# Optimization experiments

Measured on AMD Instinct MI355X. Metric: run time of the kernel, lower is better.

The kernel has to match this reference:

```python
import jax, jax.numpy as jnp
import numpy as np

N = 200000          # graph_size (stalk rows)
H = 128             # hidden_channels
NNZ = 3200000       # Laplacian nnz (avg degree 16)
K = 15              # polynomial degree (poly_layers_K)
LAMBDA_MAX = 2.0    # normalised Laplacian -> analytic lambda_max


def setup_inputs() -> dict:
    key = jax.random.key(0)
    ks = jax.random.split(key, 6)
    x = jax.random.normal(ks[0], (N, H), dtype=jnp.float32)
    vals = jax.random.normal(ks[1], (NNZ,), dtype=jnp.float32)
    poly_logits = jax.random.normal(ks[2], (K + 1,), dtype=jnp.float32)
    hp_alpha = jax.random.normal(ks[3], (), dtype=jnp.float32)
    edge_row = jax.random.randint(ks[4], (NNZ,), 0, N, dtype=jnp.int64)
    edge_col = jax.random.randint(ks[5], (NNZ,), 0, N, dtype=jnp.int64)
    return {"x": x, "vals": vals, "poly_logits": poly_logits,
            "hp_alpha": hp_alpha, "edge_row": edge_row, "edge_col": edge_col}


def reference(x, vals, poly_logits, hp_alpha, edge_row, edge_col):
    n = x.shape[0]

    def spmm(v):  # (n,h) -> (n,h), sparse L @ v in COO form
        return jax.ops.segment_sum(vals[:, None] * v[edge_col], edge_row,
                                   num_segments=n)

    def Lhat(v):  # L_hat = (2/lambda_max) L - I
        return (2.0 / LAMBDA_MAX) * spmm(v) - v

    w = jax.nn.softmax(poly_logits)  # mixture over Chebyshev T_0..T_K

    # Chebyshev Type-1 recurrence: T_{k+1} = 2 L_hat T_k - T_{k-1}
    T0 = x
    T1 = Lhat(x)
    out = w[0] * T0 + w[1] * T1

    def step(carry, wk):
        T0, T1, out = carry
        Tk1 = 2.0 * Lhat(T1) - T0
        return (T1, Tk1, out + wk * Tk1), None

    (_, _, px), _ = jax.lax.scan(step, (T0, T1, out), w[2:])

    # high-pass term: x - (1/lambda_max) L x
    hp = x - spmm(x) / LAMBDA_MAX
    return -px + hp_alpha * hp
```

## Files before the change

### kernel.cpp

```cpp
#include <hip/hip_runtime.h>
#include <math.h>

#define N_NODES 200000
#define H_CH    128
#define GRP     64
#define NNZ_E   3200000
#define K_DEG   15

__global__ void softmax_k(const float* __restrict__ logits, float* __restrict__ w) {
    if (threadIdx.x == 0) {
        float m = -1e30f;
        for (int i = 0; i <= K_DEG; ++i) m = fmaxf(m, logits[i]);
        float e[K_DEG + 1];
        float s = 0.f;
        for (int i = 0; i <= K_DEG; ++i) { e[i] = expf(logits[i] - m); s += e[i]; }
        float inv = 1.0f / s;
        for (int i = 0; i <= K_DEG; ++i) w[i] = e[i] * inv;
    }
}

__global__ void hist_k(const int* __restrict__ row, int* __restrict__ counts, int nnz) {
    int i = blockIdx.x * blockDim.x + threadIdx.x;
    if (i < nnz) atomicAdd(&counts[row[i]], 1);
}

__global__ void scan1_k(const int* __restrict__ counts, int* __restrict__ out,
                        int* __restrict__ partials, int n) {
    __shared__ int sm[256];
    int tbase = blockIdx.x * 2048 + threadIdx.x * 8;
    int v[8];
    int tsum = 0;
#pragma unroll
    for (int j = 0; j < 8; ++j) {
        int i = tbase + j;
        int c = (i < n) ? counts[i] : 0;
        v[j] = tsum;
        tsum += c;
    }
    sm[threadIdx.x] = tsum;
    __syncthreads();
    int incl = tsum;
    for (int off = 1; off < 256; off <<= 1) {
        int t = (threadIdx.x >= (unsigned)off) ? sm[threadIdx.x - off] : 0;
        __syncthreads();
        incl += t;
        sm[threadIdx.x] = incl;
        __syncthreads();
    }
    int texcl = incl - tsum;
    if (threadIdx.x == 255) partials[blockIdx.x] = incl;
#pragma unroll
    for (int j = 0; j < 8; ++j) {
        int i = tbase + j;
        if (i < n) out[i] = texcl + v[j];
    }
}

__global__ void scan2_k(int* partials, int nb, int* row_ptr, int n, int total) {
    __shared__ int sm[128];
    int v = (threadIdx.x < (unsigned)nb) ? partials[threadIdx.x] : 0;
    sm[threadIdx.x] = v;
    __syncthreads();
    int incl = v;
    for (int off = 1; off < 128; off <<= 1) {
        int t = (threadIdx.x >= (unsigned)off) ? sm[threadIdx.x - off] : 0;
        __syncthreads();
        incl += t;
        sm[threadIdx.x] = incl;
        __syncthreads();
    }
    if (threadIdx.x < (unsigned)nb) partials[threadIdx.x] = incl - v;
    if (threadIdx.x == 0) row_ptr[n] = total;
}

__global__ void scan3_k(int* __restrict__ row_ptr, const int* __restrict__ partials,
                        int* __restrict__ fill, int n) {
    int off = partials[blockIdx.x];
    int tbase = blockIdx.x * 2048 + threadIdx.x * 8;
#pragma unroll
    for (int j = 0; j < 8; ++j) {
        int i = tbase + j;
        if (i < n) {
            int v = row_ptr[i] + off;
            row_ptr[i] = v;
            fill[i] = v;
        }
    }
}

__global__ void scatter_k(const int* __restrict__ row, const int* __restrict__ col,
                          const float* __restrict__ vals, int* __restrict__ fill,
                          int2* __restrict__ csr, int nnz) {
    int i = blockIdx.x * blockDim.x + threadIdx.x;
    if (i < nnz) {
        int r = row[i];
        int p = atomicAdd(&fill[r], 1);
        int2 cv;
        cv.x = col[i];
        cv.y = __float_as_int(vals[i]);
        csr[p] = cv;
    }
}

__global__ __launch_bounds__(256) void first_k(
    const int* __restrict__ rp, const int2* __restrict__ csr,
    const float* __restrict__ x, float* __restrict__ T1g, float* __restrict__ out,
    const float* __restrict__ w, const float* __restrict__ alpha_p, int goff) {
    int wid = blockIdx.x * 4 + (threadIdx.x >> 6);
    int r = __builtin_amdgcn_readfirstlane(wid);
    if (r >= N_NODES) return;
    int lane = threadIdx.x & 63;
    const float* base = x + goff + lane;
    int e0 = rp[r], e1 = rp[r + 1];
    float a0 = 0.f, a1 = 0.f, a2 = 0.f, a3 = 0.f;
    int e = e0;
    for (; e + 4 <= e1; e += 4) {
        int2 cv0 = csr[e], cv1 = csr[e + 1], cv2 = csr[e + 2], cv3 = csr[e + 3];
        a0 = fmaf(__int_as_float(cv0.y), base[(size_t)cv0.x * H_CH], a0);
        a1 = fmaf(__int_as_float(cv1.y), base[(size_t)cv1.x * H_CH], a1);
        a2 = fmaf(__int_as_float(cv2.y), base[(size_t)cv2.x * H_CH], a2);
        a3 = fmaf(__int_as_float(cv3.y), base[(size_t)cv3.x * H_CH], a3);
    }
    for (; e < e1; ++e) {
        int2 cv = csr[e];
        a0 = fmaf(__int_as_float(cv.y), base[(size_t)cv.x * H_CH], a0);
    }
    float s = (a0 + a1) + (a2 + a3);
    size_t idxg = (size_t)r * GRP + lane;
    size_t idxf = (size_t)r * H_CH + goff + lane;
    float xr = x[idxf];
    float w0 = w[0], w1 = w[1], al = alpha_p[0];
    float t1 = s - xr;
    float o = -(w0 * xr + w1 * t1) + al * (xr - 0.5f * s);
    T1g[idxg] = t1;
    out[idxf] = o;
}

__global__ __launch_bounds__(256) void cheb_k(
    const int* __restrict__ rp, const int2* __restrict__ csr,
    const float* __restrict__ Tcur, const float* TprevBase, int tprevStride,
    float* Tnext, float* __restrict__ out,
    const float* __restrict__ w, int k, int goff) {
    int wid = blockIdx.x * 4 + (threadIdx.x >> 6);
    int r = __builtin_amdgcn_readfirstlane(wid);
    if (r >= N_NODES) return;
    int lane = threadIdx.x & 63;
    const float* base = Tcur + lane;
    int e0 = rp[r], e1 = rp[r + 1];
    float a0 = 0.f, a1 = 0.f, a2 = 0.f, a3 = 0.f;
    int e = e0;
    for (; e + 4 <= e1; e += 4) {
        int2 cv0 = csr[e], cv1 = csr[e + 1], cv2 = csr[e + 2], cv3 = csr[e + 3];
        a0 = fmaf(__int_as_float(cv0.y), base[(size_t)cv0.x * GRP], a0);
        a1 = fmaf(__int_as_float(cv1.y), base[(size_t)cv1.x * GRP], a1);
        a2 = fmaf(__int_as_float(cv2.y), base[(size_t)cv2.x * GRP], a2);
        a3 = fmaf(__int_as_float(cv3.y), base[(size_t)cv3.x * GRP], a3);
    }
    for (; e < e1; ++e) {
        int2 cv = csr[e];
        a0 = fmaf(__int_as_float(cv.y), base[(size_t)cv.x * GRP], a0);
    }
    float s = (a0 + a1) + (a2 + a3);
    size_t idxg = (size_t)r * GRP + lane;
    size_t idxf = (size_t)r * H_CH + goff + lane;
    float tc = Tcur[idxg];
    float tp = TprevBase[(size_t)r * tprevStride + lane];
    float wk = w[k];
    float tn = 2.0f * (s - tc) - tp;
    float o = out[idxf];
    o -= wk * tn;
    out[idxf] = o;
    Tnext[idxg] = tn;
}

extern "C" void kernel_launch(void* const* d_in, const int* in_sizes, int n_in,
                              void* d_out, int out_size, void* d_ws, size_t ws_size,
                              hipStream_t stream) {
    const float* x      = (const float*)d_in[0];
    const float* vals   = (const float*)d_in[1];
    const float* logits = (const float*)d_in[2];
    const float* alpha  = (const float*)d_in[3];
    const int*   erow   = (const int*)d_in[4];
    const int*   ecol   = (const int*)d_in[5];
    float* out = (float*)d_out;

    const size_t NG = (size_t)N_NODES * GRP;
    float* bufA    = (float*)d_ws;
    float* bufB    = bufA + NG;
    int2*  csr     = (int2*)(bufB + NG);
    int*   row_ptr = (int*)(csr + NNZ_E);
    int*   counts  = row_ptr + (N_NODES + 1);
    int*   fill    = counts + N_NODES;
    int*   partials= fill + N_NODES;
    float* w_buf   = (float*)(partials + 128);

    hipMemsetAsync(counts, 0, N_NODES * sizeof(int), stream);
    softmax_k<<<1, 64, 0, stream>>>(logits, w_buf);
    hist_k<<<(NNZ_E + 255) / 256, 256, 0, stream>>>(erow, counts, NNZ_E);

    const int TILE = 2048;
    int nblk = (N_NODES + TILE - 1) / TILE;
    scan1_k<<<nblk, 256, 0, stream>>>(counts, row_ptr, partials, N_NODES);
    scan2_k<<<1, 128, 0, stream>>>(partials, nblk, row_ptr, N_NODES, NNZ_E);
    scan3_k<<<nblk, 256, 0, stream>>>(row_ptr, partials, fill, N_NODES);
    scatter_k<<<(NNZ_E + 255) / 256, 256, 0, stream>>>(erow, ecol, vals, fill, csr, NNZ_E);

    int grid = (N_NODES + 3) / 4;

    for (int g = 0; g < H_CH / GRP; ++g) {
        int goff = g * GRP;
        first_k<<<grid, 256, 0, stream>>>(row_ptr, csr, x, bufB, out, w_buf, alpha, goff);
        cheb_k<<<grid, 256, 0, stream>>>(row_ptr, csr, bufB, x + goff, H_CH, bufA,
                                         out, w_buf, 2, goff);
        float* Tcur = bufA;
        float* Tprev = bufB;
        for (int k = 3; k <= K_DEG; ++k) {
            cheb_k<<<grid, 256, 0, stream>>>(row_ptr, csr, Tcur, Tprev, GRP, Tprev,
                                             out, w_buf, k, goff);
            float* t = Tcur; Tcur = Tprev; Tprev = t;
        }
    }
}
```

Before: 4.703 ms.

## Sort rows by degree, precompute scatter ranks, unroll SpMM gather by eight

Records each edge's rank within its row during the histogram pass, so the scatter no longer needs a second atomic pass over a fill array. Adds a degree bucketing pass that builds a permutation ordering rows from high to low degree, and the SpMM kernels process rows in that order to balance wave work. Widens the inner gather loop to eight independent accumulators for more loads in flight. In exchange, the permuted row order loses locality in the output and T writes, and the new rank buffer adds extra memory traffic.

```diff
diff --git a/kernel.cpp b/kernel.cpp
--- a/kernel.cpp
+++ b/kernel.cpp
@@ -6,6 +6,7 @@
 #define GRP     64
 #define NNZ_E   3200000
 #define K_DEG   15
+#define DEG_BINS 64
 
 __global__ void softmax_k(const float* __restrict__ logits, float* __restrict__ w) {
     if (threadIdx.x == 0) {
@@ -19,9 +20,10 @@
     }
 }
 
-__global__ void hist_k(const int* __restrict__ row, int* __restrict__ counts, int nnz) {
-    int i = blockIdx.x * blockDim.x + threadIdx.x;
-    if (i < nnz) atomicAdd(&counts[row[i]], 1);
+__global__ void rank_k(const int* __restrict__ row, int* __restrict__ counts,
+                       int* __restrict__ rank, int nnz) {
+    int i = blockIdx.x * blockDim.x + threadIdx.x;
+    if (i < nnz) rank[i] = atomicAdd(&counts[row[i]], 1);
 }
 
 __global__ void scan1_k(const int* __restrict__ counts, int* __restrict__ out,
@@ -73,28 +75,23 @@
     if (threadIdx.x == 0) row_ptr[n] = total;
 }
 
-__global__ void scan3_k(int* __restrict__ row_ptr, const int* __restrict__ partials,
-                        int* __restrict__ fill, int n) {
+__global__ void scan3_k(int* __restrict__ row_ptr, const int* __restrict__ partials, int n) {
     int off = partials[blockIdx.x];
     int tbase = blockIdx.x * 2048 + threadIdx.x * 8;
 #pragma unroll
     for (int j = 0; j < 8; ++j) {
         int i = tbase + j;
-        if (i < n) {
-            int v = row_ptr[i] + off;
-            row_ptr[i] = v;
-            fill[i] = v;
-        }
-    }
-}
-
-__global__ void scatter_k(const int* __restrict__ row, const int* __restrict__ col,
-                          const float* __restrict__ vals, int* __restrict__ fill,
-                          int2* __restrict__ csr, int nnz) {
+        if (i < n) row_ptr[i] += off;
+    }
+}
+
+__global__ void scatter2_k(const int* __restrict__ row, const int* __restrict__ col,
+                           const float* __restrict__ vals, const int* __restrict__ rank,
+                           const int* __restrict__ row_ptr, int2* __restrict__ csr, int nnz) {
     int i = blockIdx.x * blockDim.x + threadIdx.x;
     if (i < nnz) {
         int r = row[i];
-        int p = atomicAdd(&fill[r], 1);
+        int p = row_ptr[r] + rank[i];
         int2 cv;
         cv.x = col[i];
         cv.y = __float_as_int(vals[i]);
@@ -102,30 +99,75 @@
     }
 }
 
+__global__ void dhist_k(const int* __restrict__ counts, int* __restrict__ dhist, int n) {
+    __shared__ int h[DEG_BINS];
+    if (threadIdx.x < DEG_BINS) h[threadIdx.x] = 0;
+    __syncthreads();
+    int i = blockIdx.x * blockDim.x + threadIdx.x;
+    if (i < n) {
+        int d = counts[i];
+        int b = (d < DEG_BINS) ? (DEG_BINS - 1 - d) : 0;
+        atomicAdd(&h[b], 1);
+    }
+    __syncthreads();
+    if (threadIdx.x < DEG_BINS) atomicAdd(&dhist[threadIdx.x], h[threadIdx.x]);
+}
+
+__global__ void dscan_k(const int* __restrict__ dhist, int* __restrict__ dbase) {
+    if (threadIdx.x == 0) {
+        int s = 0;
+        for (int b = 0; b < DEG_BINS; ++b) { dbase[b] = s; s += dhist[b]; }
+    }
+}
+
+__global__ void dperm_k(const int* __restrict__ counts, const int* __restrict__ dbase,
+                        int* __restrict__ dcount, int* __restrict__ perm, int n) {
+    int i = blockIdx.x * blockDim.x + threadIdx.x;
+    if (i < n) {
+        int d = counts[i];
+        int b = (d < DEG_BINS) ? (DEG_BINS - 1 - d) : 0;
+        int p = dbase[b] + atomicAdd(&dcount[b], 1);
+        perm[p] = i;
+    }
+}
+
 __global__ __launch_bounds__(256) void first_k(
-    const int* __restrict__ rp, const int2* __restrict__ csr,
+    const int* __restrict__ rp, const int2* __restrict__ csr, const int* __restrict__ perm,
     const float* __restrict__ x, float* __restrict__ T1g, float* __restrict__ out,
     const float* __restrict__ w, const float* __restrict__ alpha_p, int goff) {
     int wid = blockIdx.x * 4 + (threadIdx.x >> 6);
-    int r = __builtin_amdgcn_readfirstlane(wid);
-    if (r >= N_NODES) return;
+    if (wid >= N_NODES) return;
+    int r = __builtin_amdgcn_readfirstlane(perm[wid]);
     int lane = threadIdx.x & 63;
     const float* base = x + goff + lane;
     int e0 = rp[r], e1 = rp[r + 1];
     float a0 = 0.f, a1 = 0.f, a2 = 0.f, a3 = 0.f;
+    float a4 = 0.f, a5 = 0.f, a6 = 0.f, a7 = 0.f;
     int e = e0;
+    for (; e + 8 <= e1; e += 8) {
+        int2 c0 = csr[e],     c1 = csr[e + 1], c2 = csr[e + 2], c3 = csr[e + 3];
+        int2 c4 = csr[e + 4], c5 = csr[e + 5], c6 = csr[e + 6], c7 = csr[e + 7];
+        a0 = fmaf(__int_as_float(c0.y), base[(size_t)c0.x * H_CH], a0);
+        a1 = fmaf(__int_as_float(c1.y), base[(size_t)c1.x * H_CH], a1);
+        a2 = fmaf(__int_as_float(c2.y), base[(size_t)c2.x * H_CH], a2);
+        a3 = fmaf(__int_as_float(c3.y), base[(size_t)c3.x * H_CH], a3);
+        a4 = fmaf(__int_as_float(c4.y), base[(size_t)c4.x * H_CH], a4);
+        a5 = fmaf(__int_as_float(c5.y), base[(size_t)c5.x * H_CH], a5);
+        a6 = fmaf(__int_as_float(c6.y), base[(size_t)c6.x * H_CH], a6);
+        a7 = fmaf(__int_as_float(c7.y), base[(size_t)c7.x * H_CH], a7);
+    }
     for (; e + 4 <= e1; e += 4) {
-        int2 cv0 = csr[e], cv1 = csr[e + 1], cv2 = csr[e + 2], cv3 = csr[e + 3];
-        a0 = fmaf(__int_as_float(cv0.y), base[(size_t)cv0.x * H_CH], a0);
-        a1 = fmaf(__int_as_float(cv1.y), base[(size_t)cv1.x * H_CH], a1);
-        a2 = fmaf(__int_as_float(cv2.y), base[(size_t)cv2.x * H_CH], a2);
-        a3 = fmaf(__int_as_float(cv3.y), base[(size_t)cv3.x * H_CH], a3);
+        int2 c0 = csr[e], c1 = csr[e + 1], c2 = csr[e + 2], c3 = csr[e + 3];
+        a0 = fmaf(__int_as_float(c0.y), base[(size_t)c0.x * H_CH], a0);
+        a1 = fmaf(__int_as_float(c1.y), base[(size_t)c1.x * H_CH], a1);
+        a2 = fmaf(__int_as_float(c2.y), base[(size_t)c2.x * H_CH], a2);
+        a3 = fmaf(__int_as_float(c3.y), base[(size_t)c3.x * H_CH], a3);
     }
     for (; e < e1; ++e) {
         int2 cv = csr[e];
         a0 = fmaf(__int_as_float(cv.y), base[(size_t)cv.x * H_CH], a0);
     }
-    float s = (a0 + a1) + (a2 + a3);
+    float s = ((a0 + a1) + (a2 + a3)) + ((a4 + a5) + (a6 + a7));
     size_t idxg = (size_t)r * GRP + lane;
     size_t idxf = (size_t)r * H_CH + goff + lane;
     float xr = x[idxf];
@@ -137,30 +179,43 @@
 }
 
 __global__ __launch_bounds__(256) void cheb_k(
-    const int* __restrict__ rp, const int2* __restrict__ csr,
+    const int* __restrict__ rp, const int2* __restrict__ csr, const int* __restrict__ perm,
     const float* __restrict__ Tcur, const float* TprevBase, int tprevStride,
     float* Tnext, float* __restrict__ out,
     const float* __restrict__ w, int k, int goff) {
     int wid = blockIdx.x * 4 + (threadIdx.x >> 6);
-    int r = __builtin_amdgcn_readfirstlane(wid);
-    if (r >= N_NODES) return;
+    if (wid >= N_NODES) return;
+    int r = __builtin_amdgcn_readfirstlane(perm[wid]);
     int lane = threadIdx.x & 63;
     const float* base = Tcur + lane;
     int e0 = rp[r], e1 = rp[r + 1];
     float a0 = 0.f, a1 = 0.f, a2 = 0.f, a3 = 0.f;
+    float a4 = 0.f, a5 = 0.f, a6 = 0.f, a7 = 0.f;
     int e = e0;
+    for (; e + 8 <= e1; e += 8) {
+        int2 c0 = csr[e],     c1 = csr[e + 1], c2 = csr[e + 2], c3 = csr[e + 3];
+        int2 c4 = csr[e + 4], c5 = csr[e + 5], c6 = csr[e + 6], c7 = csr[e + 7];
+        a0 = fmaf(__int_as_float(c0.y), base[(size_t)c0.x * GRP], a0);
+        a1 = fmaf(__int_as_float(c1.y), base[(size_t)c1.x * GRP], a1);
+        a2 = fmaf(__int_as_float(c2.y), base[(size_t)c2.x * GRP], a2);
+        a3 = fmaf(__int_as_float(c3.y), base[(size_t)c3.x * GRP], a3);
+        a4 = fmaf(__int_as_float(c4.y), base[(size_t)c4.x * GRP], a4);
+        a5 = fmaf(__int_as_float(c5.y), base[(size_t)c5.x * GRP], a5);
+        a6 = fmaf(__int_as_float(c6.y), base[(size_t)c6.x * GRP], a6);
+        a7 = fmaf(__int_as_float(c7.y), base[(size_t)c7.x * GRP], a7);
+    }
     for (; e + 4 <= e1; e += 4) {
-        int2 cv0 = csr[e], cv1 = csr[e + 1], cv2 = csr[e + 2], cv3 = csr[e + 3];
-        a0 = fmaf(__int_as_float(cv0.y), base[(size_t)cv0.x * GRP], a0);
-        a1 = fmaf(__int_as_float(cv1.y), base[(size_t)cv1.x * GRP], a1);
-        a2 = fmaf(__int_as_float(cv2.y), base[(size_t)cv2.x * GRP], a2);
-        a3 = fmaf(__int_as_float(cv3.y), base[(size_t)cv3.x * GRP], a3);
+        int2 c0 = csr[e], c1 = csr[e + 1], c2 = csr[e + 2], c3 = csr[e + 3];
+        a0 = fmaf(__int_as_float(c0.y), base[(size_t)c0.x * GRP], a0);
+        a1 = fmaf(__int_as_float(c1.y), base[(size_t)c1.x * GRP], a1);
+        a2 = fmaf(__int_as_float(c2.y), base[(size_t)c2.x * GRP], a2);
+        a3 = fmaf(__int_as_float(c3.y), base[(size_t)c3.x * GRP], a3);
     }
     for (; e < e1; ++e) {
         int2 cv = csr[e];
         a0 = fmaf(__int_as_float(cv.y), base[(size_t)cv.x * GRP], a0);
     }
-    float s = (a0 + a1) + (a2 + a3);
+    float s = ((a0 + a1) + (a2 + a3)) + ((a4 + a5) + (a6 + a7));
     size_t idxg = (size_t)r * GRP + lane;
     size_t idxf = (size_t)r * H_CH + goff + lane;
     float tc = Tcur[idxg];
@@ -190,32 +245,45 @@
     int2*  csr     = (int2*)(bufB + NG);
     int*   row_ptr = (int*)(csr + NNZ_E);
     int*   counts  = row_ptr + (N_NODES + 1);
-    int*   fill    = counts + N_NODES;
-    int*   partials= fill + N_NODES;
-    float* w_buf   = (float*)(partials + 128);
+    int*   rank    = counts + N_NODES;
+    int*   perm    = rank + NNZ_E;
+    int*   partials= perm + N_NODES;
+    int*   dhist   = partials + 128;
+    int*   dbase   = dhist + DEG_BINS;
+    int*   dcount  = dbase + DEG_BINS;
+    float* w_buf   = (float*)(dcount + DEG_BINS);
 
     hipMemsetAsync(counts, 0, N_NODES * sizeof(int), stream);
+    hipMemsetAsync(dhist, 0, DEG_BINS * sizeof(int), stream);
+    hipMemsetAsync(dcount, 0, DEG_BINS * sizeof(int), stream);
     softmax_k<<<1, 64, 0, stream>>>(logits, w_buf);
-    hist_k<<<(NNZ_E + 255) / 256, 256, 0, stream>>>(erow, counts, NNZ_E);
+
+    rank_k<<<(NNZ_E + 255) / 256, 256, 0, stream>>>(erow, counts, rank, NNZ_E);
 
     const int TILE = 2048;
     int nblk = (N_NODES + TILE - 1) / TILE;
     scan1_k<<<nblk, 256, 0, stream>>>(counts, row_ptr, partials, N_NODES);
     scan2_k<<<1, 128, 0, stream>>>(partials, nblk, row_ptr, N_NODES, NNZ_E);
-    scan3_k<<<nblk, 256, 0, stream>>>(row_ptr, partials, fill, N_NODES);
-    scatter_k<<<(NNZ_E + 255) / 256, 256, 0, stream>>>(erow, ecol, vals, fill, csr, NNZ_E);
+    scan3_k<<<nblk, 256, 0, stream>>>(row_ptr, partials, N_NODES);
+
+    dhist_k<<<(N_NODES + 255) / 256, 256, 0, stream>>>(counts, dhist, N_NODES);
+    dscan_k<<<1, 64, 0, stream>>>(dhist, dbase);
+    dperm_k<<<(N_NODES + 255) / 256, 256, 0, stream>>>(counts, dbase, dcount, perm, N_NODES);
+
+    scatter2_k<<<(NNZ_E + 255) / 256, 256, 0, stream>>>(erow, ecol, vals, rank, row_ptr,
+                                                        csr, NNZ_E);
 
     int grid = (N_NODES + 3) / 4;
 
     for (int g = 0; g < H_CH / GRP; ++g) {
         int goff = g * GRP;
-        first_k<<<grid, 256, 0, stream>>>(row_ptr, csr, x, bufB, out, w_buf, alpha, goff);
-        cheb_k<<<grid, 256, 0, stream>>>(row_ptr, csr, bufB, x + goff, H_CH, bufA,
+        first_k<<<grid, 256, 0, stream>>>(row_ptr, csr, perm, x, bufB, out, w_buf, alpha, goff);
+        cheb_k<<<grid, 256, 0, stream>>>(row_ptr, csr, perm, bufB, x + goff, H_CH, bufA,
                                          out, w_buf, 2, goff);
         float* Tcur = bufA;
         float* Tprev = bufB;
         for (int k = 3; k <= K_DEG; ++k) {
-            cheb_k<<<grid, 256, 0, stream>>>(row_ptr, csr, Tcur, Tprev, GRP, Tprev,
+            cheb_k<<<grid, 256, 0, stream>>>(row_ptr, csr, perm, Tcur, Tprev, GRP, Tprev,
                                              out, w_buf, k, goff);
             float* t = Tcur; Tcur = Tprev; Tprev = t;
         }
```

Result: slower. 5.387 ms (+14.5%).
